# Optimization experiments

Measured on AMD Instinct MI355X. Metric: run time of the kernel, lower is better.

Reference implementation:

```python
import jax, jax.numpy as jnp
import numpy as np

NEG_SLOPE = 0.2  # PyG GATConv default LeakyReLU slope


def gat_layer(x, src, dst, W, a_src, a_dst, bias, heads, out_dim, concat, n_nodes):
    # x: [N, F_in]; W: [F_in, heads*out_dim]
    h = (x @ W).reshape(n_nodes, heads, out_dim)          # [N, H, C]
    alpha_src = jnp.sum(h * a_src, axis=-1)               # [N, H]
    alpha_dst = jnp.sum(h * a_dst, axis=-1)               # [N, H]
    e = jax.nn.leaky_relu(alpha_src[src] + alpha_dst[dst], NEG_SLOPE)  # [E, H]
    # softmax over edges grouped by destination node (self-loops guarantee nonempty segments)
    m = jax.ops.segment_max(e, dst, num_segments=n_nodes)  # [N, H]
    w = jnp.exp(e - m[dst])
    s = jax.ops.segment_sum(w, dst, num_segments=n_nodes)  # [N, H]
    alpha = w / s[dst]                                     # [E, H]
    msg = h[src] * alpha[:, :, None]                       # [E, H, C]
    out = jax.ops.segment_sum(msg, dst, num_segments=n_nodes)  # [N, H, C]
    if concat:
        out = out.reshape(n_nodes, heads * out_dim)
    else:
        out = out.mean(axis=1)
    return out + bias


def setup_inputs() -> dict:
    key = jax.random.key(0)
    ks = jax.random.split(key, 12)
    N, E = 50000, 600000
    F_IN, OUT = 256, 64
    H1, C1 = 2, 2 * OUT          # conv1: heads=2, per-head dim 128
    F2 = H1 * C1                 # 256
    x = jax.random.normal(ks[0], (N, F_IN), dtype=jnp.float32)
    edge_index = jax.random.randint(ks[1], (2, E), 0, N, dtype=jnp.int64)
    g1 = 1.0 / np.sqrt(F_IN)
    g2 = 1.0 / np.sqrt(F2)
    return {
        "x": x,
        "edge_index": edge_index,
        "W1": jax.random.normal(ks[2], (F_IN, H1 * C1), dtype=jnp.float32) * g1,
        "a1_src": jax.random.normal(ks[3], (H1, C1), dtype=jnp.float32) * g2,
        "a1_dst": jax.random.normal(ks[4], (H1, C1), dtype=jnp.float32) * g2,
        "b1": jnp.zeros((H1 * C1,), dtype=jnp.float32),
        "W2": jax.random.normal(ks[5], (F2, OUT), dtype=jnp.float32) * g2,
        "a2_src": jax.random.normal(ks[6], (1, OUT), dtype=jnp.float32) * 0.1,
        "a2_dst": jax.random.normal(ks[7], (1, OUT), dtype=jnp.float32) * 0.1,
        "b2": jnp.zeros((OUT,), dtype=jnp.float32),
    }


def reference(x, edge_index, W1, a1_src, a1_dst, b1, W2, a2_src, a2_dst, b2):
    N = x.shape[0]
    # add self-loops (PyG GATConv default)
    loops = jnp.arange(N, dtype=edge_index.dtype)
    src = jnp.concatenate([edge_index[0], loops])
    dst = jnp.concatenate([edge_index[1], loops])
    OUT = W2.shape[1]
    h = gat_layer(x, src, dst, W1, a1_src, a1_dst, b1,
                  heads=2, out_dim=2 * OUT, concat=True, n_nodes=N)
    h = jax.nn.elu(h)
    out = gat_layer(h, src, dst, W2, a2_src, a2_dst, b2,
                    heads=1, out_dim=OUT, concat=False, n_nodes=N)
    return out
```

## Files before the change

### kernel.cpp

```cpp
#include <hip/hip_runtime.h>
#include <hip/hip_bf16.h>
#include <math.h>


#define NSLOPE 0.2f

using bf16x8 = __attribute__((ext_vector_type(8))) short;
using f32x4  = __attribute__((ext_vector_type(4))) float;
using u16x8  = __attribute__((ext_vector_type(8))) unsigned short;
using u16x4  = __attribute__((ext_vector_type(4))) unsigned short;

__device__ __forceinline__ unsigned short bf16_rne(float f) {
    unsigned u = __float_as_uint(f);
    return (unsigned short)((u + 0x7FFFu + ((u >> 16) & 1u)) >> 16);
}
__device__ __forceinline__ float bf16_to_f(unsigned short h) {
    return __uint_as_float(((unsigned)h) << 16);
}

__global__ __launch_bounds__(256) void k_prep_all(const float* __restrict__ x,
                                                  const float* __restrict__ W1,
                                                  const float* __restrict__ W2,
                                                  const int* __restrict__ edst,
                                                  unsigned short* __restrict__ Xhi,
                                                  unsigned short* __restrict__ Xlo,
                                                  unsigned short* __restrict__ W1hi,
                                                  unsigned short* __restrict__ W1lo,
                                                  unsigned short* __restrict__ W2hi,
                                                  unsigned short* __restrict__ W2lo,
                                                  int* __restrict__ deg,
                                                  int BX, int total4, int E) {
    int b = blockIdx.x, t = threadIdx.x;
    if (b < BX) {
        int id = b * 256 + t;
        if (id >= total4) return;
        float4 v = *(const float4*)&x[(size_t)id * 4];
        float vv[4] = {v.x, v.y, v.z, v.w};
        unsigned short hi[4], lo[4];
#pragma unroll
        for (int c = 0; c < 4; ++c) {
            unsigned short h = bf16_rne(vv[c]);
            hi[c] = h;
            lo[c] = bf16_rne(vv[c] - bf16_to_f(h));
        }
        *(u16x4*)&Xhi[(size_t)id * 4] = *(u16x4*)hi;
        *(u16x4*)&Xlo[(size_t)id * 4] = *(u16x4*)lo;
    } else if (b < BX + 64) {
        int id = (b - BX) * 256 + t;
        int n = id >> 6, kg = id & 63;
        unsigned short hi[4], lo[4];
#pragma unroll
        for (int c = 0; c < 4; ++c) {
            float w = W1[(kg * 4 + c) * 256 + n];
            unsigned short h = bf16_rne(w);
            hi[c] = h;
            lo[c] = bf16_rne(w - bf16_to_f(h));
        }
        *(u16x4*)&W1hi[n * 256 + kg * 4] = *(u16x4*)hi;
        *(u16x4*)&W1lo[n * 256 + kg * 4] = *(u16x4*)lo;
    } else if (b < BX + 128) {
        int id = (b - BX - 64) * 256 + t;
        int n = id >> 8, k = id & 255;
        float w = W2[k * 64 + n];
        unsigned short h = bf16_rne(w);
        W2hi[n * 256 + k] = h;
        W2lo[n * 256 + k] = bf16_rne(w - bf16_to_f(h));
    } else {
        int i = (b - BX - 128) * 256 + t;
        if (i < E) atomicAdd(&deg[edst[i]], 1);
    }
}

__global__ __launch_bounds__(256) void k_scan_ab(const int* __restrict__ deg,
                                                 int* __restrict__ part,
                                                 int* __restrict__ ticket,
                                                 int* __restrict__ off_n,
                                                 int n, int CH) {
    __shared__ int sd[256];
    __shared__ int lastflag;
    int b = blockIdx.x, t = threadIdx.x;
    int s = b * CH, e = min(n, s + CH);
    int loc = 0;
    for (int i = s + t; i < e; i += 256) loc += deg[i] + 1;
    sd[t] = loc;
    __syncthreads();
    for (int o = 128; o > 0; o >>= 1) {
        if (t < o) sd[t] += sd[t + o];
        __syncthreads();
    }
    if (t == 0) {
        part[b] = sd[0];
        __threadfence();
        int old = atomicAdd(ticket, 1);
        lastflag = (old == (int)gridDim.x - 1);
    }
    __syncthreads();
    if (lastflag) {
        __threadfence();
        int v = ((volatile int*)part)[t];
        sd[t] = v;
        __syncthreads();
        for (int o = 1; o < 256; o <<= 1) {
            int u = (t >= o) ? sd[t - o] : 0;
            __syncthreads();
            sd[t] += u;
            __syncthreads();
        }
        part[t] = sd[t] - v;
        if (t == 255) *off_n = sd[255];
    }
}

__global__ __launch_bounds__(256) void k_scan_c(const int* __restrict__ deg,
                                                const int* __restrict__ part,
                                                int* __restrict__ off,
                                                int* __restrict__ cur,
                                                int* __restrict__ srcl, int n, int CH) {
    __shared__ int sd[256];
    int b = blockIdx.x, t = threadIdx.x;
    int s = b * CH, e = min(n, s + CH);
    int base = part[b];
    for (int c = s; c < e; c += 256) {
        int i = c + t;
        int v = (i < e) ? (deg[i] + 1) : 0;
        sd[t] = v;
        __syncthreads();
        for (int o = 1; o < 256; o <<= 1) {
            int u = (t >= o) ? sd[t - o] : 0;
            __syncthreads();
            sd[t] += u;
            __syncthreads();
        }
        if (i < e) {
            int ex = base + sd[t] - v;
            off[i] = ex;
            cur[i] = ex + 1;
            srcl[ex] = i;
        }
        base += sd[255];
        __syncthreads();
    }
}

__global__ void k_fill(const int* __restrict__ src, const int* __restrict__ dst,
                       int* cur, int* __restrict__ srcl, int E) {
    int i = blockIdx.x * blockDim.x + threadIdx.x;
    if (i >= E) return;
    int s = src[i], d = dst[i];
    int p = atomicAdd(&cur[d], 1);
    srcl[p] = s;
}

#define G1S 40
__global__ __launch_bounds__(256) void k_gemm1(const unsigned short* __restrict__ Xhi,
                                               const unsigned short* __restrict__ Xlo,
                                               const unsigned short* __restrict__ Whi,
                                               const unsigned short* __restrict__ Wlo,
                                               const float* __restrict__ a1s,
                                               const float* __restrict__ a1d,
                                               unsigned short* __restrict__ h1b,
                                               float* __restrict__ as_,
                                               float* __restrict__ ad_, int M) {
    __shared__ unsigned short sAh[128 * G1S], sAl[128 * G1S];
    __shared__ unsigned short sBh[128 * G1S], sBl[128 * G1S];
    __shared__ float salS[128][2], salD[128][2];
    int t = threadIdx.x;
    int lane = t & 63, wave = t >> 6;
    int q = lane >> 4, m = lane & 15;
    int row0 = blockIdx.x * 128;
    int head = blockIdx.y;
    int col0 = head * 128;
    int rbase = (wave & 1) * 64, cbase = (wave >> 1) * 64;
    f32x4 acc[4][4];
#pragma unroll
    for (int i = 0; i < 4; ++i)
#pragma unroll
        for (int j = 0; j < 4; ++j) acc[i][j] = (f32x4){0.f, 0.f, 0.f, 0.f};

    for (int kc = 0; kc < 256; kc += 32) {
#pragma unroll
        for (int i = 0; i < 2; ++i) {
            int slot = t + i * 256;
            int r = slot >> 2, kg = slot & 3;
            int row = row0 + r;
            u16x8 vh = {0, 0, 0, 0, 0, 0, 0, 0};
            u16x8 vl = {0, 0, 0, 0, 0, 0, 0, 0};
            if (row < M) {
                vh = *(const u16x8*)&Xhi[(size_t)row * 256 + kc + kg * 8];
                vl = *(const u16x8*)&Xlo[(size_t)row * 256 + kc + kg * 8];
            }
            *(u16x8*)&sAh[r * G1S + kg * 8] = vh;
            *(u16x8*)&sAl[r * G1S + kg * 8] = vl;
        }
#pragma unroll
        for (int i = 0; i < 2; ++i) {
            int slot = t + i * 256;
            int n = slot >> 2, kg = slot & 3;
            *(u16x8*)&sBh[n * G1S + kg * 8] =
                *(const u16x8*)&Whi[(size_t)(col0 + n) * 256 + kc + kg * 8];
            *(u16x8*)&sBl[n * G1S + kg * 8] =
                *(const u16x8*)&Wlo[(size_t)(col0 + n) * 256 + kc + kg * 8];
        }
        __syncthreads();
        bf16x8 ah[4], al[4], bh[4], bl[4];
#pragma unroll
        for (int i = 0; i < 4; ++i) {
            int r = (rbase + i * 16 + m) * G1S + q * 8;
            ah[i] = *(bf16x8*)&sAh[r];
            al[i] = *(bf16x8*)&sAl[r];
        }
#pragma unroll
        for (int j = 0; j < 4; ++j) {
            int r = (cbase + j * 16 + m) * G1S + q * 8;
            bh[j] = *(bf16x8*)&sBh[r];
            bl[j] = *(bf16x8*)&sBl[r];
        }
#pragma unroll
        for (int i = 0; i < 4; ++i)
#pragma unroll
            for (int j = 0; j < 4; ++j) {
                acc[i][j] = __builtin_amdgcn_mfma_f32_16x16x32_bf16(ah[i], bl[j], acc[i][j], 0, 0, 0);
                acc[i][j] = __builtin_amdgcn_mfma_f32_16x16x32_bf16(al[i], bh[j], acc[i][j], 0, 0, 0);
                acc[i][j] = __builtin_amdgcn_mfma_f32_16x16x32_bf16(ah[i], bh[j], acc[i][j], 0, 0, 0);
            }
        __syncthreads();
    }
    float sv[4], dv[4];
#pragma unroll
    for (int j = 0; j < 4; ++j) {
        sv[j] = a1s[head * 128 + cbase + j * 16 + m];
        dv[j] = a1d[head * 128 + cbase + j * 16 + m];
    }
#pragma unroll
    for (int i = 0; i < 4; ++i) {
#pragma unroll
        for (int r = 0; r < 4; ++r) {
            int rl = rbase + i * 16 + q * 4 + r;
            int row = row0 + rl;
            float ps = acc[i][0][r] * sv[0] + acc[i][1][r] * sv[1]
                     + acc[i][2][r] * sv[2] + acc[i][3][r] * sv[3];
            float pd = acc[i][0][r] * dv[0] + acc[i][1][r] * dv[1]
                     + acc[i][2][r] * dv[2] + acc[i][3][r] * dv[3];
#pragma unroll
            for (int mask = 1; mask < 16; mask <<= 1) {
                ps += __shfl_xor(ps, mask, 64);
                pd += __shfl_xor(pd, mask, 64);
            }
            if (m == 0) {
                salS[rl][cbase >> 6] = ps;
                salD[rl][cbase >> 6] = pd;
            }
            if (row < M) {
#pragma unroll
                for (int j = 0; j < 4; ++j)
                    h1b[(size_t)row * 256 + col0 + cbase + j * 16 + m] = bf16_rne(acc[i][j][r]);
            }
        }
    }
    __syncthreads();
    if (t < 128) {
        int row = row0 + t;
        if (row < M) {
            as_[row * 2 + head] = salS[t][0] + salS[t][1];
            ad_[row * 2 + head] = salD[t][0] + salD[t][1];
        }
    }
}

__global__ __launch_bounds__(256) void k_agg1(const unsigned short* __restrict__ h1b,
                                              const float* __restrict__ as,
                                              const float* __restrict__ ad,
                                              const int* __restrict__ off,
                                              const int* __restrict__ srcl,
                                              const float* __restrict__ b1,
                                              unsigned short* __restrict__ helu_b, int N) {
    int wid = (blockIdx.x * blockDim.x + threadIdx.x) >> 6;
    int lane = threadIdx.x & 63;
    if (wid >= N) return;
    int p0 = off[wid], p1 = off[wid + 1];
    float ad0 = ad[wid * 2], ad1 = ad[wid * 2 + 1];
    int half = lane >> 5, hl = lane & 31;
    int headL = hl >> 4;
    float acc[8];
#pragma unroll
    for (int c = 0; c < 8; ++c) acc[c] = 0.f;
    float sumw = 0.f;
    for (int base = p0; base < p1; base += 64) {
        int p = base + lane;
        int cnt = min(64, p1 - base);
        int s = 0; float w0 = 0.f, w1 = 0.f;
        if (p < p1) {
            s = srcl[p];
            float2 av = *(const float2*)&as[s * 2];
            float l0 = av.x + ad0; l0 = l0 >= 0.f ? l0 : NSLOPE * l0;
            float l1 = av.y + ad1; l1 = l1 >= 0.f ? l1 : NSLOPE * l1;
            w0 = __expf(l0); w1 = __expf(l1);
        }
        int pairs = (cnt + 1) >> 1;
        int jj = 0;
        for (; jj + 2 <= pairs; jj += 2) {
            int e0 = 2 * jj + half, e1 = e0 + 2;
            int sa = __shfl(s, e0, 64), sb = __shfl(s, e1, 64);
            float wa0 = __shfl(w0, e0, 64), wa1 = __shfl(w1, e0, 64);
            float wb0 = __shfl(w0, e1, 64), wb1 = __shfl(w1, e1, 64);
            u16x8 hva = *(const u16x8*)&h1b[(size_t)sa * 256 + hl * 8];
            u16x8 hvb = *(const u16x8*)&h1b[(size_t)sb * 256 + hl * 8];
            float wa = headL ? wa1 : wa0;
            float wb = headL ? wb1 : wb0;
            sumw += wa + wb;
#pragma unroll
            for (int c = 0; c < 8; ++c)
                acc[c] += wa * bf16_to_f(hva[c]) + wb * bf16_to_f(hvb[c]);
        }
        for (; jj < pairs; ++jj) {
            int e0 = 2 * jj + half;
            int sa = __shfl(s, e0, 64);
            float wa0 = __shfl(w0, e0, 64), wa1 = __shfl(w1, e0, 64);
            u16x8 hva = *(const u16x8*)&h1b[(size_t)sa * 256 + hl * 8];
            float wa = headL ? wa1 : wa0;
            sumw += wa;
#pragma unroll
            for (int c = 0; c < 8; ++c) acc[c] += wa * bf16_to_f(hva[c]);
        }
    }
#pragma unroll
    for (int c = 0; c < 8; ++c) acc[c] += __shfl_xor(acc[c], 32, 64);
    sumw += __shfl_xor(sumw, 32, 64);
    float inv = 1.0f / sumw;
    int ch = hl * 8 + half * 4;
    float4 bv = *(const float4*)&b1[ch];
    float bb[4] = {bv.x, bv.y, bv.z, bv.w};
    unsigned short o[4];
#pragma unroll
    for (int c = 0; c < 4; ++c) {
        float v = acc[half * 4 + c] * inv + bb[c];
        v = v > 0.f ? v : expm1f(v);
        o[c] = bf16_rne(v);
    }
    *(u16x4*)&helu_b[(size_t)wid * 256 + ch] = *(u16x4*)o;
}

__global__ __launch_bounds__(256) void k_gemm2(const unsigned short* __restrict__ hb,
                                               const unsigned short* __restrict__ Whi,
                                               const unsigned short* __restrict__ Wlo,
                                               const float* __restrict__ a2s,
                                               const float* __restrict__ a2d,
                                               unsigned short* __restrict__ h2b,
                                               float* __restrict__ as_,
                                               float* __restrict__ ad_, int M) {
    __shared__ unsigned short sA[128 * G1S];
    __shared__ unsigned short sBh[64 * G1S], sBl[64 * G1S];
    int t = threadIdx.x;
    int lane = t & 63, wave = t >> 6;
    int q = lane >> 4, m = lane & 15;
    int row0 = blockIdx.x * 128;
    int rbase = wave * 32;
    f32x4 acc[2][4];
#pragma unroll
    for (int i = 0; i < 2; ++i)
#pragma unroll
        for (int j = 0; j < 4; ++j) acc[i][j] = (f32x4){0.f, 0.f, 0.f, 0.f};

    for (int kc = 0; kc < 256; kc += 32) {
#pragma unroll
        for (int i = 0; i < 2; ++i) {
            int slot = t + i * 256;
            int r = slot >> 2, kg = slot & 3;
            int row = row0 + r;
            u16x8 v = {0, 0, 0, 0, 0, 0, 0, 0};
            if (row < M) v = *(const u16x8*)&hb[(size_t)row * 256 + kc + kg * 8];
            *(u16x8*)&sA[r * G1S + kg * 8] = v;
        }
        {
            int n = t >> 2, kg = t & 3;
            *(u16x8*)&sBh[n * G1S + kg * 8] =
                *(const u16x8*)&Whi[(size_t)n * 256 + kc + kg * 8];
            *(u16x8*)&sBl[n * G1S + kg * 8] =
                *(const u16x8*)&Wlo[(size_t)n * 256 + kc + kg * 8];
        }
        __syncthreads();
        bf16x8 a[2], bh[4], bl[4];
#pragma unroll
        for (int i = 0; i < 2; ++i)
            a[i] = *(bf16x8*)&sA[(rbase + i * 16 + m) * G1S + q * 8];
#pragma unroll
        for (int j = 0; j < 4; ++j) {
            bh[j] = *(bf16x8*)&sBh[(j * 16 + m) * G1S + q * 8];
            bl[j] = *(bf16x8*)&sBl[(j * 16 + m) * G1S + q * 8];
        }
#pragma unroll
        for (int i = 0; i < 2; ++i)
#pragma unroll
            for (int j = 0; j < 4; ++j) {
                acc[i][j] = __builtin_amdgcn_mfma_f32_16x16x32_bf16(a[i], bl[j], acc[i][j], 0, 0, 0);
                acc[i][j] = __builtin_amdgcn_mfma_f32_16x16x32_bf16(a[i], bh[j], acc[i][j], 0, 0, 0);
            }
        __syncthreads();
    }
    float sv[4], dv[4];
#pragma unroll
    for (int j = 0; j < 4; ++j) {
        sv[j] = a2s[j * 16 + m];
        dv[j] = a2d[j * 16 + m];
    }
#pragma unroll
    for (int i = 0; i < 2; ++i) {
#pragma unroll
        for (int r = 0; r < 4; ++r) {
            int row = row0 + rbase + i * 16 + q * 4 + r;
            float ps = acc[i][0][r] * sv[0] + acc[i][1][r] * sv[1]
                     + acc[i][2][r] * sv[2] + acc[i][3][r] * sv[3];
            float pd = acc[i][0][r] * dv[0] + acc[i][1][r] * dv[1]
                     + acc[i][2][r] * dv[2] + acc[i][3][r] * dv[3];
#pragma unroll
            for (int mask = 1; mask < 16; mask <<= 1) {
                ps += __shfl_xor(ps, mask, 64);
                pd += __shfl_xor(pd, mask, 64);
            }
            if (row < M) {
#pragma unroll
                for (int j = 0; j < 4; ++j)
                    h2b[(size_t)row * 64 + j * 16 + m] = bf16_rne(acc[i][j][r]);
                if (m == 0) { as_[row] = ps; ad_[row] = pd; }
            }
        }
    }
}

__global__ __launch_bounds__(256) void k_agg2(const unsigned short* __restrict__ h2b,
                                              const float* __restrict__ as,
                                              const float* __restrict__ ad,
                                              const int* __restrict__ off,
                                              const int* __restrict__ srcl,
                                              const float* __restrict__ b2,
                                              float* __restrict__ out, int N) {
    int wid = (blockIdx.x * blockDim.x + threadIdx.x) >> 6;
    int lane = threadIdx.x & 63;
    if (wid >= N) return;
    int p0 = off[wid], p1 = off[wid + 1];
    float adw = ad[wid];
    int g = lane >> 4, gl = lane & 15;
    float acc[4];
#pragma unroll
    for (int c = 0; c < 4; ++c) acc[c] = 0.f;
    float sumw = 0.f;
    for (int base = p0; base < p1; base += 64) {
        int p = base + lane;
        int cnt = min(64, p1 - base);
        int s = 0; float w = 0.f;
        if (p < p1) {
            s = srcl[p];
            float l = as[s] + adw;
            l = l >= 0.f ? l : NSLOPE * l;
            w = __expf(l);
        }
        int quads = (cnt + 3) >> 2;
        int jj = 0;
        for (; jj + 2 <= quads; jj += 2) {
            int e0 = 4 * jj + g, e1 = e0 + 4;
            int sa = __shfl(s, e0, 64), sb = __shfl(s, e1, 64);
            float wa = __shfl(w, e0, 64), wb = __shfl(w, e1, 64);
            u16x4 hva = *(const u16x4*)&h2b[(size_t)sa * 64 + gl * 4];
            u16x4 hvb = *(const u16x4*)&h2b[(size_t)sb * 64 + gl * 4];
            sumw += wa + wb;
            acc[0] += wa * bf16_to_f(hva.x) + wb * bf16_to_f(hvb.x);
            acc[1] += wa * bf16_to_f(hva.y) + wb * bf16_to_f(hvb.y);
            acc[2] += wa * bf16_to_f(hva.z) + wb * bf16_to_f(hvb.z);
            acc[3] += wa * bf16_to_f(hva.w) + wb * bf16_to_f(hvb.w);
        }
        for (; jj < quads; ++jj) {
            int e0 = 4 * jj + g;
            int sa = __shfl(s, e0, 64);
            float wa = __shfl(w, e0, 64);
            u16x4 hva = *(const u16x4*)&h2b[(size_t)sa * 64 + gl * 4];
            sumw += wa;
            acc[0] += wa * bf16_to_f(hva.x);
            acc[1] += wa * bf16_to_f(hva.y);
            acc[2] += wa * bf16_to_f(hva.z);
            acc[3] += wa * bf16_to_f(hva.w);
        }
    }
#pragma unroll
    for (int c = 0; c < 4; ++c) {
        acc[c] += __shfl_xor(acc[c], 16, 64);
        acc[c] += __shfl_xor(acc[c], 32, 64);
    }
    sumw += __shfl_xor(sumw, 16, 64);
    sumw += __shfl_xor(sumw, 32, 64);
    if (g == 0) {
        float inv = 1.0f / sumw;
        float4 bv = *(const float4*)&b2[gl * 4];
        float4 o;
        o.x = acc[0] * inv + bv.x;
        o.y = acc[1] * inv + bv.y;
        o.z = acc[2] * inv + bv.z;
        o.w = acc[3] * inv + bv.w;
        *(float4*)&out[(size_t)wid * 64 + gl * 4] = o;
    }
}

extern "C" void kernel_launch(void* const* d_in, const int* in_sizes, int n_in,
                              void* d_out, int out_size, void* d_ws, size_t ws_size,
                              hipStream_t stream) {
    if (n_in < 10) return;
    const float* x   = (const float*)d_in[0];
    const int*   ei  = (const int*)d_in[1];
    const float* W1  = (const float*)d_in[2];
    const float* a1s = (const float*)d_in[3];
    const float* a1d = (const float*)d_in[4];
    const float* b1  = (const float*)d_in[5];
    const float* W2  = (const float*)d_in[6];
    const float* a2s = (const float*)d_in[7];
    const float* a2d = (const float*)d_in[8];
    const float* b2  = (const float*)d_in[9];
    float* out = (float*)d_out;

    const int N = in_sizes[0] / 256;
    const int E = in_sizes[1] / 2;
    const int T = E + N;
    const int* esrc = ei;
    const int* edst = ei + E;

    char* ws = (char*)d_ws;
    size_t o = 0;
    auto alloc = [&](size_t bytes) -> void* {
        void* p = ws + o;
        o = (o + bytes + 255) & ~(size_t)255;
        return p;
    };
    size_t szX = (size_t)N * 256 * 2;
    char* regionA = (char*)alloc(2 * szX);
    unsigned short* Xhi = (unsigned short*)regionA;
    unsigned short* Xlo = (unsigned short*)(regionA + szX);
    unsigned short* helu_b = (unsigned short*)regionA;

    unsigned short* h1b  = (unsigned short*)alloc((size_t)N * 256 * 2);
    unsigned short* W1hi = (unsigned short*)alloc(256 * 256 * 2);
    unsigned short* W1lo = (unsigned short*)alloc(256 * 256 * 2);
    unsigned short* W2hi = (unsigned short*)alloc(64 * 256 * 2);
    unsigned short* W2lo = (unsigned short*)alloc(64 * 256 * 2);
    unsigned short* h2b  = (unsigned short*)alloc((size_t)N * 64 * 2);
    float* al1s = (float*)alloc((size_t)N * 2 * 4);
    float* al1d = (float*)alloc((size_t)N * 2 * 4);
    float* al2s = (float*)alloc((size_t)N * 4);
    float* al2d = (float*)alloc((size_t)N * 4);
    int* deg  = (int*)alloc((size_t)(N + 64) * 4);
    int* ticket = deg + N;
    int* off  = (int*)alloc((size_t)(N + 1) * 4);
    int* cur  = (int*)alloc((size_t)N * 4);
    int* part = (int*)alloc(256 * 4);
    int* srcl = (int*)alloc((size_t)T * 4);
    if (o > ws_size) return;

    const int CH = (N + 255) / 256;
    const int total4 = N * 64;
    const int BX = (total4 + 255) / 256;
    const int BH = (E + 255) / 256;

    hipMemsetAsync(deg, 0, (size_t)(N + 64) * 4, stream);
    k_prep_all<<<BX + 128 + BH, 256, 0, stream>>>(x, W1, W2, edst, Xhi, Xlo,
                                                  W1hi, W1lo, W2hi, W2lo, deg,
                                                  BX, total4, E);
    k_scan_ab<<<256, 256, 0, stream>>>(deg, part, ticket, &off[N], N, CH);
    k_scan_c<<<256, 256, 0, stream>>>(deg, part, off, cur, srcl, N, CH);
    k_fill<<<(E + 255) / 256, 256, 0, stream>>>(esrc, edst, cur, srcl, E);

    dim3 g1((N + 127) / 128, 2);
    k_gemm1<<<g1, 256, 0, stream>>>(Xhi, Xlo, W1hi, W1lo, a1s, a1d, h1b, al1s, al1d, N);
    k_agg1<<<(N + 3) / 4, 256, 0, stream>>>(h1b, al1s, al1d, off, srcl, b1, helu_b, N);

    k_gemm2<<<(N + 127) / 128, 256, 0, stream>>>(helu_b, W2hi, W2lo, a2s, a2d, h2b, al2s, al2d, N);
    k_agg2<<<(N + 3) / 4, 256, 0, stream>>>(h2b, al2s, al2d, off, srcl, b2, out, N);
}
```

Before: 301.1 us.

## Fuse x bf16 hi/lo split into gemm1 and compute both heads per block

The separate pass that splits x into bf16 hi/lo arrays is removed, and gemm1 now loads fp32 x directly and does the split while staging tiles into shared memory. Each block now covers both heads (256 output columns) instead of using a 2-wide grid, so x is read once rather than twice, and each wave owns one head, which lets the attention-logit reduction skip the shared-memory exchange. This drops a 50000x256 read/write round trip. In exchange the accumulator grows to 4x8 tiles (register pressure, lower occupancy), the B tile in shared memory doubles, and the grid halves.

```diff
diff --git a/kernel.cpp b/kernel.cpp
--- a/kernel.cpp
+++ b/kernel.cpp
@@ -18,35 +18,17 @@
     return __uint_as_float(((unsigned)h) << 16);
 }
 
-__global__ __launch_bounds__(256) void k_prep_all(const float* __restrict__ x,
-                                                  const float* __restrict__ W1,
+__global__ __launch_bounds__(256) void k_prep_all(const float* __restrict__ W1,
                                                   const float* __restrict__ W2,
                                                   const int* __restrict__ edst,
-                                                  unsigned short* __restrict__ Xhi,
-                                                  unsigned short* __restrict__ Xlo,
                                                   unsigned short* __restrict__ W1hi,
                                                   unsigned short* __restrict__ W1lo,
                                                   unsigned short* __restrict__ W2hi,
                                                   unsigned short* __restrict__ W2lo,
-                                                  int* __restrict__ deg,
-                                                  int BX, int total4, int E) {
+                                                  int* __restrict__ deg, int E) {
     int b = blockIdx.x, t = threadIdx.x;
-    if (b < BX) {
+    if (b < 64) {
         int id = b * 256 + t;
-        if (id >= total4) return;
-        float4 v = *(const float4*)&x[(size_t)id * 4];
-        float vv[4] = {v.x, v.y, v.z, v.w};
-        unsigned short hi[4], lo[4];
-#pragma unroll
-        for (int c = 0; c < 4; ++c) {
-            unsigned short h = bf16_rne(vv[c]);
-            hi[c] = h;
-            lo[c] = bf16_rne(vv[c] - bf16_to_f(h));
-        }
-        *(u16x4*)&Xhi[(size_t)id * 4] = *(u16x4*)hi;
-        *(u16x4*)&Xlo[(size_t)id * 4] = *(u16x4*)lo;
-    } else if (b < BX + 64) {
-        int id = (b - BX) * 256 + t;
         int n = id >> 6, kg = id & 63;
         unsigned short hi[4], lo[4];
 #pragma unroll
@@ -58,15 +40,15 @@
         }
         *(u16x4*)&W1hi[n * 256 + kg * 4] = *(u16x4*)hi;
         *(u16x4*)&W1lo[n * 256 + kg * 4] = *(u16x4*)lo;
-    } else if (b < BX + 128) {
-        int id = (b - BX - 64) * 256 + t;
+    } else if (b < 128) {
+        int id = (b - 64) * 256 + t;
         int n = id >> 8, k = id & 255;
         float w = W2[k * 64 + n];
         unsigned short h = bf16_rne(w);
         W2hi[n * 256 + k] = h;
         W2lo[n * 256 + k] = bf16_rne(w - bf16_to_f(h));
     } else {
-        int i = (b - BX - 128) * 256 + t;
+        int i = (b - 128) * 256 + t;
         if (i < E) atomicAdd(&deg[edst[i]], 1);
     }
 }
@@ -152,8 +134,7 @@
 }
 
 #define G1S 40
-__global__ __launch_bounds__(256) void k_gemm1(const unsigned short* __restrict__ Xhi,
-                                               const unsigned short* __restrict__ Xlo,
+__global__ __launch_bounds__(256) void k_gemm1(const float* __restrict__ x,
                                                const unsigned short* __restrict__ Whi,
                                                const unsigned short* __restrict__ Wlo,
                                                const float* __restrict__ a1s,
@@ -162,47 +143,50 @@
                                                float* __restrict__ as_,
                                                float* __restrict__ ad_, int M) {
     __shared__ unsigned short sAh[128 * G1S], sAl[128 * G1S];
-    __shared__ unsigned short sBh[128 * G1S], sBl[128 * G1S];
-    __shared__ float salS[128][2], salD[128][2];
+    __shared__ unsigned short sBh[256 * G1S], sBl[256 * G1S];
     int t = threadIdx.x;
     int lane = t & 63, wave = t >> 6;
     int q = lane >> 4, m = lane & 15;
     int row0 = blockIdx.x * 128;
-    int head = blockIdx.y;
-    int col0 = head * 128;
-    int rbase = (wave & 1) * 64, cbase = (wave >> 1) * 64;
-    f32x4 acc[4][4];
+    int rbase = (wave & 1) * 64;
+    int head = wave >> 1;
+    int cb = head * 128;
+    f32x4 acc[4][8];
 #pragma unroll
     for (int i = 0; i < 4; ++i)
 #pragma unroll
-        for (int j = 0; j < 4; ++j) acc[i][j] = (f32x4){0.f, 0.f, 0.f, 0.f};
+        for (int j = 0; j < 8; ++j) acc[i][j] = (f32x4){0.f, 0.f, 0.f, 0.f};
 
     for (int kc = 0; kc < 256; kc += 32) {
 #pragma unroll
-        for (int i = 0; i < 2; ++i) {
-            int slot = t + i * 256;
-            int r = slot >> 2, kg = slot & 3;
+        for (int i2 = 0; i2 < 4; ++i2) {
+            int slot = t + i2 * 256;
+            int r = slot >> 3, kg = slot & 7;
             int row = row0 + r;
-            u16x8 vh = {0, 0, 0, 0, 0, 0, 0, 0};
-            u16x8 vl = {0, 0, 0, 0, 0, 0, 0, 0};
-            if (row < M) {
-                vh = *(const u16x8*)&Xhi[(size_t)row * 256 + kc + kg * 8];
-                vl = *(const u16x8*)&Xlo[(size_t)row * 256 + kc + kg * 8];
-            }
-            *(u16x8*)&sAh[r * G1S + kg * 8] = vh;
-            *(u16x8*)&sAl[r * G1S + kg * 8] = vl;
-        }
-#pragma unroll
-        for (int i = 0; i < 2; ++i) {
-            int slot = t + i * 256;
+            float4 v = make_float4(0.f, 0.f, 0.f, 0.f);
+            if (row < M) v = *(const float4*)&x[(size_t)row * 256 + kc + kg * 4];
+            float vv[4] = {v.x, v.y, v.z, v.w};
+            unsigned short hi[4], lo[4];
+#pragma unroll
+            for (int c = 0; c < 4; ++c) {
+                unsigned short h = bf16_rne(vv[c]);
+                hi[c] = h;
+                lo[c] = bf16_rne(vv[c] - bf16_to_f(h));
+            }
+            *(u16x4*)&sAh[r * G1S + kg * 4] = *(u16x4*)hi;
+            *(u16x4*)&sAl[r * G1S + kg * 4] = *(u16x4*)lo;
+        }
+#pragma unroll
+        for (int i2 = 0; i2 < 4; ++i2) {
+            int slot = t + i2 * 256;
             int n = slot >> 2, kg = slot & 3;
             *(u16x8*)&sBh[n * G1S + kg * 8] =
-                *(const u16x8*)&Whi[(size_t)(col0 + n) * 256 + kc + kg * 8];
+                *(const u16x8*)&Whi[(size_t)n * 256 + kc + kg * 8];
             *(u16x8*)&sBl[n * G1S + kg * 8] =
-                *(const u16x8*)&Wlo[(size_t)(col0 + n) * 256 + kc + kg * 8];
-        }
-        __syncthreads();
-        bf16x8 ah[4], al[4], bh[4], bl[4];
+                *(const u16x8*)&Wlo[(size_t)n * 256 + kc + kg * 8];
+        }
+        __syncthreads();
+        bf16x8 ah[4], al[4];
 #pragma unroll
         for (int i = 0; i < 4; ++i) {
             int r = (rbase + i * 16 + m) * G1S + q * 8;
@@ -210,59 +194,50 @@
             al[i] = *(bf16x8*)&sAl[r];
         }
 #pragma unroll
-        for (int j = 0; j < 4; ++j) {
-            int r = (cbase + j * 16 + m) * G1S + q * 8;
-            bh[j] = *(bf16x8*)&sBh[r];
-            bl[j] = *(bf16x8*)&sBl[r];
-        }
-#pragma unroll
-        for (int i = 0; i < 4; ++i)
-#pragma unroll
-            for (int j = 0; j < 4; ++j) {
-                acc[i][j] = __builtin_amdgcn_mfma_f32_16x16x32_bf16(ah[i], bl[j], acc[i][j], 0, 0, 0);
-                acc[i][j] = __builtin_amdgcn_mfma_f32_16x16x32_bf16(al[i], bh[j], acc[i][j], 0, 0, 0);
-                acc[i][j] = __builtin_amdgcn_mfma_f32_16x16x32_bf16(ah[i], bh[j], acc[i][j], 0, 0, 0);
-            }
-        __syncthreads();
-    }
-    float sv[4], dv[4];
-#pragma unroll
-    for (int j = 0; j < 4; ++j) {
-        sv[j] = a1s[head * 128 + cbase + j * 16 + m];
-        dv[j] = a1d[head * 128 + cbase + j * 16 + m];
+        for (int j = 0; j < 8; ++j) {
+            int rB = (cb + j * 16 + m) * G1S + q * 8;
+            bf16x8 bhj = *(bf16x8*)&sBh[rB];
+            bf16x8 blj = *(bf16x8*)&sBl[rB];
+#pragma unroll
+            for (int i = 0; i < 4; ++i) {
+                acc[i][j] = __builtin_amdgcn_mfma_f32_16x16x32_bf16(ah[i], blj, acc[i][j], 0, 0, 0);
+                acc[i][j] = __builtin_amdgcn_mfma_f32_16x16x32_bf16(al[i], bhj, acc[i][j], 0, 0, 0);
+                acc[i][j] = __builtin_amdgcn_mfma_f32_16x16x32_bf16(ah[i], bhj, acc[i][j], 0, 0, 0);
+            }
+        }
+        __syncthreads();
+    }
+    float sv[8], dv[8];
+#pragma unroll
+    for (int j = 0; j < 8; ++j) {
+        sv[j] = a1s[head * 128 + j * 16 + m];
+        dv[j] = a1d[head * 128 + j * 16 + m];
     }
 #pragma unroll
     for (int i = 0; i < 4; ++i) {
 #pragma unroll
         for (int r = 0; r < 4; ++r) {
-            int rl = rbase + i * 16 + q * 4 + r;
-            int row = row0 + rl;
-            float ps = acc[i][0][r] * sv[0] + acc[i][1][r] * sv[1]
-                     + acc[i][2][r] * sv[2] + acc[i][3][r] * sv[3];
-            float pd = acc[i][0][r] * dv[0] + acc[i][1][r] * dv[1]
-                     + acc[i][2][r] * dv[2] + acc[i][3][r] * dv[3];
+            int row = row0 + rbase + i * 16 + q * 4 + r;
+            float ps = 0.f, pd = 0.f;
+#pragma unroll
+            for (int j = 0; j < 8; ++j) {
+                ps += acc[i][j][r] * sv[j];
+                pd += acc[i][j][r] * dv[j];
+            }
 #pragma unroll
             for (int mask = 1; mask < 16; mask <<= 1) {
                 ps += __shfl_xor(ps, mask, 64);
                 pd += __shfl_xor(pd, mask, 64);
             }
-            if (m == 0) {
-                salS[rl][cbase >> 6] = ps;
-                salD[rl][cbase >> 6] = pd;
-            }
             if (row < M) {
 #pragma unroll
-                for (int j = 0; j < 4; ++j)
-                    h1b[(size_t)row * 256 + col0 + cbase + j * 16 + m] = bf16_rne(acc[i][j][r]);
-            }
-        }
-    }
-    __syncthreads();
-    if (t < 128) {
-        int row = row0 + t;
-        if (row < M) {
-            as_[row * 2 + head] = salS[t][0] + salS[t][1];
-            ad_[row * 2 + head] = salD[t][0] + salD[t][1];
+                for (int j = 0; j < 8; ++j)
+                    h1b[(size_t)row * 256 + head * 128 + j * 16 + m] = bf16_rne(acc[i][j][r]);
+                if (m == 0) {
+                    as_[row * 2 + head] = ps;
+                    ad_[row * 2 + head] = pd;
+                }
+            }
         }
     }
 }
@@ -528,18 +503,13 @@
         o = (o + bytes + 255) & ~(size_t)255;
         return p;
     };
-    size_t szX = (size_t)N * 256 * 2;
-    char* regionA = (char*)alloc(2 * szX);
-    unsigned short* Xhi = (unsigned short*)regionA;
-    unsigned short* Xlo = (unsigned short*)(regionA + szX);
-    unsigned short* helu_b = (unsigned short*)regionA;
-
-    unsigned short* h1b  = (unsigned short*)alloc((size_t)N * 256 * 2);
-    unsigned short* W1hi = (unsigned short*)alloc(256 * 256 * 2);
-    unsigned short* W1lo = (unsigned short*)alloc(256 * 256 * 2);
-    unsigned short* W2hi = (unsigned short*)alloc(64 * 256 * 2);
-    unsigned short* W2lo = (unsigned short*)alloc(64 * 256 * 2);
-    unsigned short* h2b  = (unsigned short*)alloc((size_t)N * 64 * 2);
+    unsigned short* h1b    = (unsigned short*)alloc((size_t)N * 256 * 2);
+    unsigned short* helu_b = (unsigned short*)alloc((size_t)N * 256 * 2);
+    unsigned short* W1hi   = (unsigned short*)alloc(256 * 256 * 2);
+    unsigned short* W1lo   = (unsigned short*)alloc(256 * 256 * 2);
+    unsigned short* W2hi   = (unsigned short*)alloc(64 * 256 * 2);
+    unsigned short* W2lo   = (unsigned short*)alloc(64 * 256 * 2);
+    unsigned short* h2b    = (unsigned short*)alloc((size_t)N * 64 * 2);
     float* al1s = (float*)alloc((size_t)N * 2 * 4);
     float* al1d = (float*)alloc((size_t)N * 2 * 4);
     float* al2s = (float*)alloc((size_t)N * 4);
@@ -553,22 +523,20 @@
     if (o > ws_size) return;
 
     const int CH = (N + 255) / 256;
-    const int total4 = N * 64;
-    const int BX = (total4 + 255) / 256;
     const int BH = (E + 255) / 256;
 
     hipMemsetAsync(deg, 0, (size_t)(N + 64) * 4, stream);
-    k_prep_all<<<BX + 128 + BH, 256, 0, stream>>>(x, W1, W2, edst, Xhi, Xlo,
-                                                  W1hi, W1lo, W2hi, W2lo, deg,
-                                                  BX, total4, E);
+    k_prep_all<<<128 + BH, 256, 0, stream>>>(W1, W2, edst, W1hi, W1lo,
+                                             W2hi, W2lo, deg, E);
     k_scan_ab<<<256, 256, 0, stream>>>(deg, part, ticket, &off[N], N, CH);
     k_scan_c<<<256, 256, 0, stream>>>(deg, part, off, cur, srcl, N, CH);
     k_fill<<<(E + 255) / 256, 256, 0, stream>>>(esrc, edst, cur, srcl, E);
 
-    dim3 g1((N + 127) / 128, 2);
-    k_gemm1<<<g1, 256, 0, stream>>>(Xhi, Xlo, W1hi, W1lo, a1s, a1d, h1b, al1s, al1d, N);
+    k_gemm1<<<(N + 127) / 128, 256, 0, stream>>>(x, W1hi, W1lo, a1s, a1d,
+                                                 h1b, al1s, al1d, N);
     k_agg1<<<(N + 3) / 4, 256, 0, stream>>>(h1b, al1s, al1d, off, srcl, b1, helu_b, N);
 
-    k_gemm2<<<(N + 127) / 128, 256, 0, stream>>>(helu_b, W2hi, W2lo, a2s, a2d, h2b, al2s, al2d, N);
+    k_gemm2<<<(N + 127) / 128, 256, 0, stream>>>(helu_b, W2hi, W2lo, a2s, a2d,
+                                                 h2b, al2s, al2d, N);
     k_agg2<<<(N + 3) / 4, 256, 0, stream>>>(h2b, al2s, al2d, off, srcl, b2, out, N);
 }
```

Measured after the change: 317.6 us. 5.5% more time.
